# Performance work log

Hardware: AMD Instinct MI355X
Metric: run time of the kernel (lower is better)

## Reference

```python
import jax, jax.numpy as jnp
import numpy as np

B, T, F, H = 4096, 128, 64, 32
SCALE = 0.05  # small init so relu-LSTM doesn't blow up over 128 steps


def setup_inputs() -> dict:
    key = jax.random.key(0)
    ks = jax.random.split(key, 7)
    return {
        "x": jax.random.normal(ks[0], (B, T, F), jnp.float32),
        "We": jax.random.normal(ks[1], (F, 4 * H), jnp.float32) * SCALE,
        "Ue": jax.random.normal(ks[2], (H, 4 * H), jnp.float32) * SCALE,
        "be": jnp.zeros((4 * H,), jnp.float32),
        "Wd": jax.random.normal(ks[3], (H, 4 * H), jnp.float32) * SCALE,
        "Ud": jax.random.normal(ks[4], (H, 4 * H), jnp.float32) * SCALE,
        "bd": jnp.zeros((4 * H,), jnp.float32),
        "Wout": jax.random.normal(ks[5], (H, F), jnp.float32) * SCALE,
        "bout": jnp.zeros((F,), jnp.float32),
    }


def _lstm_relu(x, W, U, b):
    """Keras LSTM with activation='relu', recurrent_activation='sigmoid'.
    x: [B,T,D]. Returns (h_T [B,H], h_seq [B,T,H]). Gate order: i,f,c,o."""
    Bx = x.shape[0]
    Hh = U.shape[0]
    xz = jnp.einsum('btd,dg->btg', x, W) + b  # precompute input projections

    def step(carry, zt):
        h, c = carry
        z = zt + h @ U
        i, f, g, o = jnp.split(z, 4, axis=-1)
        i = jax.nn.sigmoid(i)
        f = jax.nn.sigmoid(f)
        g = jax.nn.relu(g)
        o = jax.nn.sigmoid(o)
        c = f * c + i * g
        h = o * jax.nn.relu(c)
        return (h, c), h

    h0 = jnp.zeros((Bx, Hh), x.dtype)
    (hT, _), hs = jax.lax.scan(step, (h0, h0), jnp.swapaxes(xz, 0, 1))
    return hT, jnp.swapaxes(hs, 0, 1)


def reference(x, We, Ue, be, Wd, Ud, bd, Wout, bout):
    # Encoder: LSTM(32, relu, return_sequences=False) -> RepeatVector(T)
    hT, _ = _lstm_relu(x, We, Ue, be)                      # [B,H]
    z = jnp.broadcast_to(hT[:, None, :], (x.shape[0], x.shape[1], hT.shape[-1]))
    # Decoder: LSTM(32, relu, return_sequences=True) -> TimeDistributed(Dense(F))
    _, hs = _lstm_relu(z, Wd, Ud, bd)                      # [B,T,H]
    return jnp.einsum('bth,hf->btf', hs, Wout) + bout      # [B,T,F]
```

## Files before the change

kernel.cpp:

```cpp
#include <hip/hip_runtime.h>
#include <hip/hip_bf16.h>

#define B_ 4096
#define T_ 128
#define F_ 64
#define H_ 32
#define G_ 128

using short8 = __attribute__((ext_vector_type(8))) short;
using f32x4  = __attribute__((ext_vector_type(4))) float;

#define MFMA16(Af, Bf, Cf) __builtin_amdgcn_mfma_f32_16x16x32_bf16((Af), (Bf), (Cf), 0, 0, 0)

__device__ __forceinline__ float sigmoid_f(float z) {
    return __builtin_amdgcn_rcpf(1.0f + __expf(-z));
}
__device__ __forceinline__ unsigned short bfb(float f) {
    return __builtin_bit_cast(unsigned short, __float2bfloat16(f));
}

extern "C" __global__ __launch_bounds__(64, 1)
void lstm_ae(const float* __restrict__ x,
             const float* __restrict__ We,
             const float* __restrict__ Ue,
             const float* __restrict__ be,
             const float* __restrict__ Wd,
             const float* __restrict__ Ud,
             const float* __restrict__ bd,
             const float* __restrict__ Wout,
             const float* __restrict__ bout,
             float* __restrict__ out)
{
    const int lane = threadIdx.x;
    const int g = lane >> 4;
    const int c = lane & 15;
    const int b0 = blockIdx.x << 4;

    __shared__ __align__(16) unsigned short hlds[16 * 40];

    short8 weF[8][2];
    short8 ueF[8];
#pragma unroll
    for (int n = 0; n < 8; ++n) {
#pragma unroll
        for (int kc = 0; kc < 2; ++kc)
#pragma unroll
            for (int i = 0; i < 8; ++i)
                weF[n][kc][i] = (short)bfb(We[(kc * 32 + 8 * g + i) * G_ + 16 * n + c]);
#pragma unroll
        for (int i = 0; i < 8; ++i)
            ueF[n][i] = (short)bfb(Ue[(8 * g + i) * G_ + 16 * n + c]);
    }
    f32x4 beC[8];
#pragma unroll
    for (int n = 0; n < 8; ++n) {
        float v = be[16 * n + c];
        f32x4 t; t[0] = v; t[1] = v; t[2] = v; t[3] = v;
        beC[n] = t;
    }

    const float* xr = x + (size_t)(b0 + c) * (T_ * F_);
    const int xo = 8 * g;

    short8 hfrag = (short8)0;
    float cs[2][4];
#pragma unroll
    for (int jh = 0; jh < 2; ++jh)
#pragma unroll
        for (int r = 0; r < 4; ++r) cs[jh][r] = 0.f;

    f32x4 xa = *(const f32x4*)(xr + xo);
    f32x4 xb = *(const f32x4*)(xr + xo + 4);
    f32x4 xc = *(const f32x4*)(xr + 32 + xo);
    f32x4 xd = *(const f32x4*)(xr + 36 + xo);

#pragma unroll 1
    for (int t = 0; t < T_; ++t) {
        short8 xf0, xf1;
#pragma unroll
        for (int i = 0; i < 4; ++i) {
            xf0[i]     = (short)bfb(xa[i]);
            xf0[4 + i] = (short)bfb(xb[i]);
            xf1[i]     = (short)bfb(xc[i]);
            xf1[4 + i] = (short)bfb(xd[i]);
        }
        if (t + 1 < T_) {
            const float* xn = xr + (t + 1) * F_;
            xa = *(const f32x4*)(xn + xo);
            xb = *(const f32x4*)(xn + xo + 4);
            xc = *(const f32x4*)(xn + 32 + xo);
            xd = *(const f32x4*)(xn + 36 + xo);
        }

        f32x4 acc[8];
#pragma unroll
        for (int n = 0; n < 8; ++n) {
            acc[n] = MFMA16(xf0, weF[n][0], beC[n]);
            acc[n] = MFMA16(xf1, weF[n][1], acc[n]);
            acc[n] = MFMA16(hfrag, ueF[n], acc[n]);
        }

#pragma unroll
        for (int jh = 0; jh < 2; ++jh)
#pragma unroll
            for (int r = 0; r < 4; ++r) {
                float iv = sigmoid_f(acc[0 + jh][r]);
                float fv = sigmoid_f(acc[2 + jh][r]);
                float gv = fmaxf(acc[4 + jh][r], 0.f);
                float ov = sigmoid_f(acc[6 + jh][r]);
                float cc = fmaf(fv, cs[jh][r], iv * gv);
                cs[jh][r] = cc;
                float hv = ov * fmaxf(cc, 0.f);
                hlds[(4 * g + r) * 40 + c + 16 * jh] = bfb(hv);
            }
        hfrag = *(const short8*)&hlds[c * 40 + 8 * g];
    }

    short8 udF[8], woF[4];
    f32x4 zd[8], boC[4];
    {
        short8 wdF[8];
#pragma unroll
        for (int n = 0; n < 8; ++n)
#pragma unroll
            for (int i = 0; i < 8; ++i) {
                wdF[n][i] = (short)bfb(Wd[(8 * g + i) * G_ + 16 * n + c]);
                udF[n][i] = (short)bfb(Ud[(8 * g + i) * G_ + 16 * n + c]);
            }
#pragma unroll
        for (int m = 0; m < 4; ++m) {
#pragma unroll
            for (int i = 0; i < 8; ++i)
                woF[m][i] = (short)bfb(Wout[(8 * g + i) * F_ + 16 * m + c]);
            float v = bout[16 * m + c];
            f32x4 tb; tb[0] = v; tb[1] = v; tb[2] = v; tb[3] = v;
            boC[m] = tb;
        }
#pragma unroll
        for (int n = 0; n < 8; ++n) {
            float v = bd[16 * n + c];
            f32x4 tb; tb[0] = v; tb[1] = v; tb[2] = v; tb[3] = v;
            zd[n] = MFMA16(hfrag, wdF[n], tb);
        }
    }

    hfrag = (short8)0;
#pragma unroll
    for (int jh = 0; jh < 2; ++jh)
#pragma unroll
        for (int r = 0; r < 4; ++r) cs[jh][r] = 0.f;

    float* ob[4];
#pragma unroll
    for (int r = 0; r < 4; ++r)
        ob[r] = out + (size_t)(b0 + 4 * g + r) * (T_ * F_) + c;

#pragma unroll 1
    for (int t = 0; t < T_; ++t) {
        f32x4 acc[8];
#pragma unroll
        for (int n = 0; n < 8; ++n)
            acc[n] = MFMA16(hfrag, udF[n], zd[n]);

#pragma unroll
        for (int jh = 0; jh < 2; ++jh)
#pragma unroll
            for (int r = 0; r < 4; ++r) {
                float iv = sigmoid_f(acc[0 + jh][r]);
                float fv = sigmoid_f(acc[2 + jh][r]);
                float gv = fmaxf(acc[4 + jh][r], 0.f);
                float ov = sigmoid_f(acc[6 + jh][r]);
                float cc = fmaf(fv, cs[jh][r], iv * gv);
                cs[jh][r] = cc;
                float hv = ov * fmaxf(cc, 0.f);
                hlds[(4 * g + r) * 40 + c + 16 * jh] = bfb(hv);
            }
        hfrag = *(const short8*)&hlds[c * 40 + 8 * g];

        f32x4 oac[4];
#pragma unroll
        for (int m = 0; m < 4; ++m)
            oac[m] = MFMA16(hfrag, woF[m], boC[m]);
#pragma unroll
        for (int m = 0; m < 4; ++m)
#pragma unroll
            for (int r = 0; r < 4; ++r)
                ob[r][t * F_ + 16 * m] = oac[m][r];
    }
}

extern "C" void kernel_launch(void* const* d_in, const int* in_sizes, int n_in,
                              void* d_out, int out_size, void* d_ws, size_t ws_size,
                              hipStream_t stream) {
    (void)in_sizes; (void)n_in; (void)d_ws; (void)ws_size; (void)out_size;
    const float* x    = (const float*)d_in[0];
    const float* We   = (const float*)d_in[1];
    const float* Ue   = (const float*)d_in[2];
    const float* be   = (const float*)d_in[3];
    const float* Wd   = (const float*)d_in[4];
    const float* Ud   = (const float*)d_in[5];
    const float* bd   = (const float*)d_in[6];
    const float* Wout = (const float*)d_in[7];
    const float* bout = (const float*)d_in[8];
    float* out = (float*)d_out;

    dim3 grid(B_ / 16), block(64);
    hipLaunchKernelGGL(lstm_ae, grid, block, 0, stream,
                       x, We, Ue, be, Wd, Ud, bd, Wout, bout, out);
}
```

Measured before the change: 367.9 us.

## Swap MFMA operand order so gate outputs feed the next step from registers

```diff
diff --git a/kernel.cpp b/kernel.cpp
--- a/kernel.cpp
+++ b/kernel.cpp
@@ -36,8 +36,6 @@
     const int c = lane & 15;
     const int b0 = blockIdx.x << 4;
 
-    __shared__ __align__(16) unsigned short hlds[16 * 40];
-
     short8 weF[8][2];
     short8 ueF[8];
 #pragma unroll
@@ -49,15 +47,12 @@
                 weF[n][kc][i] = (short)bfb(We[(kc * 32 + 8 * g + i) * G_ + 16 * n + c]);
 #pragma unroll
         for (int i = 0; i < 8; ++i)
-            ueF[n][i] = (short)bfb(Ue[(8 * g + i) * G_ + 16 * n + c]);
+            ueF[n][i] = (short)bfb(Ue[(4 * g + (i & 3) + 16 * (i >> 2)) * G_ + 16 * n + c]);
     }
     f32x4 beC[8];
 #pragma unroll
-    for (int n = 0; n < 8; ++n) {
-        float v = be[16 * n + c];
-        f32x4 t; t[0] = v; t[1] = v; t[2] = v; t[3] = v;
-        beC[n] = t;
-    }
+    for (int n = 0; n < 8; ++n)
+        beC[n] = *(const f32x4*)(be + 16 * n + 4 * g);
 
     const float* xr = x + (size_t)(b0 + c) * (T_ * F_);
     const int xo = 8 * g;
@@ -95,9 +90,9 @@
         f32x4 acc[8];
 #pragma unroll
         for (int n = 0; n < 8; ++n) {
-            acc[n] = MFMA16(xf0, weF[n][0], beC[n]);
-            acc[n] = MFMA16(xf1, weF[n][1], acc[n]);
-            acc[n] = MFMA16(hfrag, ueF[n], acc[n]);
+            acc[n] = MFMA16(weF[n][0], xf0, beC[n]);
+            acc[n] = MFMA16(weF[n][1], xf1, acc[n]);
+            acc[n] = MFMA16(ueF[n], hfrag, acc[n]);
         }
 
 #pragma unroll
@@ -111,9 +106,8 @@
                 float cc = fmaf(fv, cs[jh][r], iv * gv);
                 cs[jh][r] = cc;
                 float hv = ov * fmaxf(cc, 0.f);
-                hlds[(4 * g + r) * 40 + c + 16 * jh] = bfb(hv);
+                hfrag[4 * jh + r] = (short)bfb(hv);
             }
-        hfrag = *(const short8*)&hlds[c * 40 + 8 * g];
     }
 
     short8 udF[8], woF[4];
@@ -124,23 +118,23 @@
         for (int n = 0; n < 8; ++n)
 #pragma unroll
             for (int i = 0; i < 8; ++i) {
-                wdF[n][i] = (short)bfb(Wd[(8 * g + i) * G_ + 16 * n + c]);
-                udF[n][i] = (short)bfb(Ud[(8 * g + i) * G_ + 16 * n + c]);
+                int pr = 4 * g + (i & 3) + 16 * (i >> 2);
+                wdF[n][i] = (short)bfb(Wd[pr * G_ + 16 * n + c]);
+                udF[n][i] = (short)bfb(Ud[pr * G_ + 16 * n + c]);
             }
 #pragma unroll
         for (int m = 0; m < 4; ++m) {
 #pragma unroll
             for (int i = 0; i < 8; ++i)
-                woF[m][i] = (short)bfb(Wout[(8 * g + i) * F_ + 16 * m + c]);
+                woF[m][i] = (short)bfb(Wout[(4 * g + (i & 3) + 16 * (i >> 2)) * F_ + 16 * m + c]);
             float v = bout[16 * m + c];
             f32x4 tb; tb[0] = v; tb[1] = v; tb[2] = v; tb[3] = v;
             boC[m] = tb;
         }
 #pragma unroll
         for (int n = 0; n < 8; ++n) {
-            float v = bd[16 * n + c];
-            f32x4 tb; tb[0] = v; tb[1] = v; tb[2] = v; tb[3] = v;
-            zd[n] = MFMA16(hfrag, wdF[n], tb);
+            f32x4 tb = *(const f32x4*)(bd + 16 * n + 4 * g);
+            zd[n] = MFMA16(wdF[n], hfrag, tb);
         }
     }
 
@@ -160,7 +154,7 @@
         f32x4 acc[8];
 #pragma unroll
         for (int n = 0; n < 8; ++n)
-            acc[n] = MFMA16(hfrag, udF[n], zd[n]);
+            acc[n] = MFMA16(udF[n], hfrag, zd[n]);
 
 #pragma unroll
         for (int jh = 0; jh < 2; ++jh)
@@ -173,9 +167,8 @@
                 float cc = fmaf(fv, cs[jh][r], iv * gv);
                 cs[jh][r] = cc;
                 float hv = ov * fmaxf(cc, 0.f);
-                hlds[(4 * g + r) * 40 + c + 16 * jh] = bfb(hv);
+                hfrag[4 * jh + r] = (short)bfb(hv);
             }
-        hfrag = *(const short8*)&hlds[c * 40 + 8 * g];
 
         f32x4 oac[4];
 #pragma unroll
```

Result: slower. 404.4 us (+9.9%).
